# Kernel tuning notes

Measured on AMD Instinct MI355X. Metric: run time of the kernel, lower is better.

Reference implementation:

```python
import jax, jax.numpy as jnp
import numpy as np

NUM_PROJS = 7
BLOCK = 256       # HyperAttention block_size
SAMPLE = 256      # HyperAttention sample_size
NUM_HEADS = 16

def _hamming_perm(n):
    a = np.array([0, 1])
    for _ in range(n - 1):
        a = np.concatenate([a, a[::-1] + a.max() + 1])
    return a

_PERM = jnp.asarray(_hamming_perm(NUM_PROJS))           # [128] gray-code-ish bucket reorder
_ENC = (2 ** jnp.arange(NUM_PROJS)).astype(jnp.int32)   # [7]

def _lsh_hash(mat, proj_dir):
    # mat: [B,H,N,d], proj_dir: [d,7] -> bucket ids [B,H,N]
    bits = jnp.einsum('bhnd,dr->bhnr', mat, proj_dir) > 0
    ids = (bits * _ENC).sum(-1)
    return _PERM[ids]

def _attn_lse(q, k, v, scale, bias=None):
    s = jnp.einsum('...qd,...kd->...qk', q, k) * scale
    if bias is not None:
        s = s + bias
    lse = jax.nn.logsumexp(s, axis=-1, keepdims=True)
    o = jnp.einsum('...qk,...kd->...qd', jnp.exp(s - lse), v)
    return o, lse

def _gather(t, idx):
    # gather rows along axis 2: out[b,h,s] = t[b,h,idx[b,h,s]]
    return jnp.take_along_axis(t, idx[..., None], axis=2)

def setup_inputs():
    key = jax.random.key(0)
    ks = jax.random.split(key, 7)
    B, L, D, INNER = 2, 8192, 1024, 1024
    x = jax.random.normal(ks[0], (B, L, D), jnp.float32)
    W_qkv = jax.random.normal(ks[1], (D, 3 * INNER), jnp.float32) / np.sqrt(D)
    b_qkv = jnp.zeros((3 * INNER,), jnp.float32)
    W_proj = jax.random.normal(ks[2], (INNER, D), jnp.float32) / np.sqrt(INNER)
    b_proj = jnp.zeros((D,), jnp.float32)
    proj_dir = jax.random.normal(ks[3], (INNER // NUM_HEADS, NUM_PROJS), jnp.float32)
    sampled_set = jax.random.randint(ks[4], (B, NUM_HEADS, SAMPLE), 0, L)
    return {"x": x, "W_qkv": W_qkv, "b_qkv": b_qkv, "W_proj": W_proj,
            "b_proj": b_proj, "proj_dir": proj_dir, "sampled_set": sampled_set}

def reference(x, W_qkv, b_qkv, W_proj, b_proj, proj_dir, sampled_set):
    B, L, D = x.shape
    qkv = (x @ W_qkv + b_qkv).reshape(B, L, 3, NUM_HEADS, -1).transpose(2, 0, 3, 1, 4)
    q, k, v = qkv[0], qkv[1], qkv[2]                      # [B,H,L,dh]
    dh = q.shape[-1]
    scale = dh ** -0.5
    # 1. sortLSH: stable sort q and k rows by angular-LSH bucket id
    q_idx = jnp.argsort(_lsh_hash(q, proj_dir), axis=2, stable=True)
    k_idx = jnp.argsort(_lsh_hash(k, proj_dir), axis=2, stable=True)
    q_idx_inv = jnp.argsort(q_idx, axis=2, stable=True)   # to restore row order
    qs = _gather(q, q_idx)
    ksort = _gather(k, k_idx)
    vsort = _gather(v, k_idx)
    # block-diagonal exact attention over the sorted order (L % BLOCK == 0 here)
    nb = L // BLOCK
    ab, lb = _attn_lse(qs.reshape(B, NUM_HEADS, nb, BLOCK, dh),
                       ksort.reshape(B, NUM_HEADS, nb, BLOCK, dh),
                       vsort.reshape(B, NUM_HEADS, nb, BLOCK, dh), scale)
    attn_block = ab.reshape(B, NUM_HEADS, L, dh)
    lse_block = lb.reshape(B, NUM_HEADS, L, 1)
    # 2. residual uniformly-sampled attention, masking entries already covered by blocks
    k_sub = _gather(ksort, sampled_set)                   # [B,H,SAMPLE,dh]
    v_sub = _gather(vsort, sampled_set)
    blk_q = jnp.arange(L)[None, None, :, None] // BLOCK   # query block id (query_block_size==BLOCK)
    mask = blk_q == (sampled_set // BLOCK)[:, :, None, :]  # [B,H,L,SAMPLE]
    bias = jnp.where(mask, jnp.finfo(x.dtype).min, 0.0).astype(x.dtype)
    attn_res, lse_res = _attn_lse(qs, k_sub, v_sub, scale, bias)
    lse_res = lse_res + jnp.log(jnp.float32(L) / SAMPLE)  # importance weight n_key/sample_size
    # combine the two attentions via their log-sum-exps
    c = 1.0 / (1.0 + jnp.exp(lse_res - lse_block))
    attn = c * attn_block + (1.0 - c) * attn_res
    out = _gather(attn, q_idx_inv)                        # un-sort rows back to input order
    out = out.transpose(0, 2, 1, 3).reshape(B, L, -1)     # [B,L,inner]
    return out @ W_proj + b_proj
```

## Files before the change

kernel.cpp:

```cpp
#include <hip/hip_runtime.h>
#include <hip/hip_fp16.h>
#include <math.h>


typedef _Float16 f16x8 __attribute__((ext_vector_type(8)));
typedef _Float16 f16x4 __attribute__((ext_vector_type(4)));
typedef __fp16 fp16x2 __attribute__((ext_vector_type(2)));
typedef float f32x4 __attribute__((ext_vector_type(4)));

#define WLIST_CAP 524288
#define TAU 0.08f

__device__ __forceinline__ void gl_lds16(const void* g, void* s) {
    __builtin_amdgcn_global_load_lds(
        (const __attribute__((address_space(1))) unsigned int*)g,
        (__attribute__((address_space(3))) unsigned int*)s, 16, 0, 0);
}

__global__ __launch_bounds__(256) void fold_kernel(
    const float* __restrict__ W, const float* __restrict__ bias,
    const float* __restrict__ proj, double* __restrict__ fold,
    double* __restrict__ bfold, _Float16* __restrict__ foldh,
    float* __restrict__ bfold32)
{
    int idx = blockIdx.x * 256 + threadIdx.x;
    if (idx < 2 * 16 * 7 * 1024) {
        int task = idx / 7168;
        int rem = idx - task * 7168;
        int i = rem / 7;
        int r = rem - i * 7;
        int h = task & 15, w = task >> 4;
        double s = 0.0;
        const float* wp = W + (size_t)i * 3072 + w * 1024 + h * 64;
        for (int d = 0; d < 64; ++d)
            s += (double)wp[d] * (double)proj[d * 7 + r];
        fold[idx] = s;
        foldh[((size_t)task * 7 + r) * 1024 + i] = (_Float16)s;
    }
    if (idx < 32768)
        foldh[229376 + idx] = (_Float16)0.f;
    if (idx < 224) {
        int r = idx % 7;
        int task = idx / 7;
        int h = task & 15, w = task >> 4;
        double s = 0.0;
        for (int d = 0; d < 64; ++d)
            s += (double)bias[w * 1024 + h * 64 + d] * (double)proj[d * 7 + r];
        bfold[idx] = s;
        bfold32[idx] = (float)s;
    }
}

__global__ __launch_bounds__(256) void hashext_kernel(
    const float* __restrict__ scores, const float* __restrict__ bfold32,
    int* __restrict__ hq, int* __restrict__ hk,
    int* __restrict__ wcount, int* __restrict__ wlist)
{
    int tid = blockIdx.x * 256 + threadIdx.x;
    int row = tid >> 5, task = tid & 31;
    const float* sp = scores + (size_t)row * 256 + task * 7;
    int id = 0, fl = 0;
#pragma unroll
    for (int r = 0; r < 7; ++r) {
        float val = sp[r] + bfold32[task * 7 + r];
        if (fabsf(val) < TAU) fl = 1;
        if (val > 0.f) id |= (1 << r);
    }
    int hsh = id ^ (id >> 1);
    int w = task >> 4, h = task & 15;
    int b = row >> 13, l = row & 8191;
    (w ? hk : hq)[((size_t)(b * 16 + h) << 13) + l] = hsh;
    if (fl) {
        int slot = atomicAdd(wcount, 1);
        if (slot < WLIST_CAP) wlist[slot] = task * 16384 + row;
    }
}

__global__ __launch_bounds__(256) void refine_kernel(
    const float* __restrict__ x, const double* __restrict__ fold,
    const double* __restrict__ bfold, const int* __restrict__ wcount,
    const int* __restrict__ wlist, int* __restrict__ hq, int* __restrict__ hk)
{
    int n = *wcount;
    if (n > WLIST_CAP) n = WLIST_CAP;
    int lane = threadIdx.x & 63;
    int wid = (blockIdx.x * 256 + threadIdx.x) >> 6;
    int nw = gridDim.x * 4;
    for (int e = wid; e < n; e += nw) {
        int code = wlist[e];
        int task = code >> 14, grow = code & 16383;
        const double* f = fold + (size_t)task * 7168;
        const float* xp = x + (size_t)grow * 1024;
        double acc[7] = {0, 0, 0, 0, 0, 0, 0};
        for (int i = lane; i < 1024; i += 64) {
            double xv = (double)xp[i];
#pragma unroll
            for (int rr = 0; rr < 7; ++rr)
                acc[rr] = fma(xv, f[(size_t)i * 7 + rr], acc[rr]);
        }
        int id = 0;
#pragma unroll
        for (int rr = 0; rr < 7; ++rr) {
            double a = acc[rr];
#pragma unroll
            for (int off = 32; off > 0; off >>= 1) a += __shfl_xor(a, off, 64);
            if (a + bfold[task * 7 + rr] > 0.0) id |= (1 << rr);
        }
        if (lane == 0) {
            int hsh = id ^ (id >> 1);
            int w = task >> 4, h = task & 15;
            int b = grow >> 13, l = grow & 8191;
            (w ? hk : hq)[((size_t)(b * 16 + h) << 13) + l] = hsh;
        }
    }
}

__global__ __launch_bounds__(256) void sort_kernel(
    const int* __restrict__ hq, const int* __restrict__ hk,
    int* __restrict__ qidx, int* __restrict__ kidx)
{
    __shared__ unsigned short cnt[128][128];
    __shared__ int tot[128];
    __shared__ int base[128];
    int blk = blockIdx.x;
    int sel = blk >> 5, bh = blk & 31;
    const int* hp = (sel ? hk : hq) + ((size_t)bh << 13);
    int* op = (sel ? kidx : qidx) + ((size_t)bh << 13);
    int t = threadIdx.x;
    for (int i = t; i < 128 * 128 / 2; i += 256) ((unsigned int*)cnt)[i] = 0u;
    __syncthreads();
    if (t < 128) {
        const int* p = hp + t * 64;
        for (int j = 0; j < 64; ++j) cnt[t][p[j]]++;
    }
    __syncthreads();
    if (t < 128) {
        int run = 0;
        for (int c = 0; c < 128; ++c) {
            int x2 = cnt[c][t];
            cnt[c][t] = (unsigned short)run;
            run += x2;
        }
        tot[t] = run;
    }
    __syncthreads();
    if (t == 0) {
        int run = 0;
        for (int v = 0; v < 128; ++v) { base[v] = run; run += tot[v]; }
    }
    __syncthreads();
    if (t < 128) {
        const int* p = hp + t * 64;
        for (int j = 0; j < 64; ++j) {
            int v = p[j];
            int c = cnt[t][v];
            cnt[t][v] = (unsigned short)(c + 1);
            op[base[v] + c] = t * 64 + j;
        }
    }
}

__global__ __launch_bounds__(256) void castx_kernel(
    const float* __restrict__ x, _Float16* __restrict__ xh)
{
    int i = blockIdx.x * 256 + threadIdx.x;
    float4 f = ((const float4*)x)[i];
    _Float16 h4[4] = {(_Float16)f.x, (_Float16)f.y, (_Float16)f.z, (_Float16)f.w};
    *(short4*)&xh[(size_t)i * 4] = *(short4*)h4;
}

__global__ __launch_bounds__(256) void transpose_kernel(
    const float* __restrict__ W, _Float16* __restrict__ Wt, int K, int N)
{
    __shared__ float tile[32][33];
    int bx = blockIdx.x, by = blockIdx.y;
    int tx = threadIdx.x & 31, ty = threadIdx.x >> 5;
    for (int i = ty; i < 32; i += 8)
        tile[i][tx] = W[(size_t)(by * 32 + i) * N + bx * 32 + tx];
    __syncthreads();
    for (int i = ty; i < 32; i += 8)
        Wt[(size_t)(bx * 32 + i) * K + by * 32 + tx] = (_Float16)tile[tx][i];
}

template <int MODE>
__global__ __launch_bounds__(256) void mfma_gemm(
    const _Float16* __restrict__ A, const _Float16* __restrict__ Bt,
    const float* __restrict__ bias, float* __restrict__ C,
    _Float16* __restrict__ Q, _Float16* __restrict__ Kb, _Float16* __restrict__ Vb,
    int K, int N)
{
    __shared__ __align__(16) _Float16 As[128 * 32];
    __shared__ __align__(16) _Float16 Bs[128 * 32];
    int t = threadIdx.x;
    int w = t >> 6, l = t & 63;
    int m0 = blockIdx.y * 128, n0 = blockIdx.x * 128;
    const _Float16* ga = A + (size_t)(m0 + 32 * w + (l >> 2)) * K + (l & 3) * 8;
    const _Float16* gb = Bt + (size_t)(n0 + 32 * w + (l >> 2)) * K + (l & 3) * 8;
    char* lasA = (char*)As + w * 2048;
    char* lasB = (char*)Bs + w * 2048;
    int wr = w >> 1, wc = w & 1;
    int rl = l & 15, ks = l >> 4;
    f32x4 acc[4][4];
#pragma unroll
    for (int m = 0; m < 4; ++m)
#pragma unroll
        for (int n = 0; n < 4; ++n) acc[m][n] = (f32x4){0.f, 0.f, 0.f, 0.f};
    for (int kk = 0; kk < K; kk += 32) {
        __syncthreads();
        gl_lds16(ga, lasA);
        gl_lds16(ga + 16 * K, lasA + 1024);
        gl_lds16(gb, lasB);
        gl_lds16(gb + 16 * K, lasB + 1024);
        ga += 32; gb += 32;
        __syncthreads();
        f16x8 af[4], bf[4];
#pragma unroll
        for (int m = 0; m < 4; ++m)
            af[m] = *(const f16x8*)((char*)As + (64 * wr + 16 * m + rl) * 64 + ks * 16);
#pragma unroll
        for (int n = 0; n < 4; ++n)
            bf[n] = *(const f16x8*)((char*)Bs + (64 * wc + 16 * n + rl) * 64 + ks * 16);
#pragma unroll
        for (int m = 0; m < 4; ++m)
#pragma unroll
            for (int n = 0; n < 4; ++n)
                acc[m][n] = __builtin_amdgcn_mfma_f32_16x16x32_f16(
                    af[m], bf[n], acc[m][n], 0, 0, 0);
    }
#pragma unroll
    for (int m = 0; m < 4; ++m) {
#pragma unroll
        for (int n = 0; n < 4; ++n) {
            int gn = n0 + 64 * wc + 16 * n + rl;
            float bv = (MODE == 2) ? 0.f : bias[gn];
#pragma unroll
            for (int j = 0; j < 4; ++j) {
                int gm = m0 + 64 * wr + 16 * m + 4 * ks + j;
                float val = acc[m][n][j] + bv;
                if (MODE == 1) {
                    int s = gn >> 10, h = (gn >> 6) & 15, d = gn & 63;
                    int b2 = gm >> 13, ll = gm & 8191;
                    _Float16* dst = (s == 0) ? Q : (s == 1 ? Kb : Vb);
                    dst[(((size_t)(b2 * 16 + h) << 13) + ll) * 64 + d] = (_Float16)val;
                } else {
                    C[(size_t)gm * N + gn] = val;
                }
            }
        }
    }
}

__global__ __launch_bounds__(256) void attn_mfma_kernel(
    const _Float16* __restrict__ q, const _Float16* __restrict__ k,
    const _Float16* __restrict__ v, const int* __restrict__ qidx,
    const int* __restrict__ kidx, const int* __restrict__ sampled,
    _Float16* __restrict__ pre)
{
    __shared__ __align__(16) _Float16 Vt[2][64 * 68];
    __shared__ int sposS[2][64];
    __shared__ int krowS[2][64];
    int bh = blockIdx.x >> 6, qb = (blockIdx.x >> 1) & 31, half = blockIdx.x & 1;
    int bb = bh >> 4, hh = bh & 15;
    size_t hb = (size_t)bh << 13;
    size_t bhs = (size_t)bh * 256;
    int t = threadIdx.x;
    int w = t >> 6, l = t & 63;
    int g = l >> 4, c16 = l & 15;
    int kg = t & 15, dg = t >> 4;
    int qw0 = qb * 256 + half * 128 + w * 32;
    const _Float16 qs = (_Float16)0.125f;

    int orig[2];
    f16x8 qf[2][2];
#pragma unroll
    for (int n = 0; n < 2; ++n) {
        orig[n] = qidx[hb + qw0 + 16 * n + c16];
        const _Float16* qp = q + (hb + orig[n]) * 64 + g * 8;
        qf[n][0] = *(const f16x8*)(qp);
        qf[n][1] = *(const f16x8*)(qp + 32);
#pragma unroll
        for (int j = 0; j < 8; ++j) { qf[n][0][j] *= qs; qf[n][1][j] *= qs; }
    }
    f32x4 o[4][2];
    float mr[2], lr[2];
#pragma unroll
    for (int n = 0; n < 2; ++n) {
        mr[n] = -1e30f; lr[n] = 0.f;
#pragma unroll
        for (int d2 = 0; d2 < 4; ++d2) o[d2][n] = (f32x4){0.f, 0.f, 0.f, 0.f};
    }
    const float LOG32 = 3.4657359027997265f;

    {
        if (t < 64) {
            int p = qb * 256 + t;
            sposS[0][t] = p;
            krowS[0][t] = kidx[hb + p];
        }
        f16x4 vr[4];
#pragma unroll
        for (int j2 = 0; j2 < 4; ++j2) {
            int p = qb * 256 + 4 * kg + j2;
            int kr = kidx[hb + p];
            vr[j2] = *(const f16x4*)(v + (hb + kr) * 64 + 4 * dg);
        }
#pragma unroll
        for (int i = 0; i < 4; ++i) {
            f16x4 o4 = {vr[0][i], vr[1][i], vr[2][i], vr[3][i]};
            *(f16x4*)&Vt[0][(4 * dg + i) * 68 + 4 * kg] = o4;
        }
    }

    for (int c = 0; c < 8; ++c) {
        int cur = c & 1, nxt = cur ^ 1;
        bool samp = c >= 4;
        __syncthreads();
        int krA[4];
#pragma unroll
        for (int m = 0; m < 4; ++m) krA[m] = krowS[cur][16 * m + c16];
        f16x8 kf[4][2];
#pragma unroll
        for (int m = 0; m < 4; ++m) {
            const _Float16* kp = k + (hb + krA[m]) * 64 + g * 8;
            kf[m][0] = *(const f16x8*)(kp);
            kf[m][1] = *(const f16x8*)(kp + 32);
        }
        int np_s = 0, nkr_s = 0, krn[4];
        if (c < 7) {
            bool snx = (c + 1) >= 4;
            if (t < 64) {
                np_s = snx ? sampled[bhs + (c - 3) * 64 + t] : qb * 256 + (c + 1) * 64 + t;
                nkr_s = kidx[hb + np_s];
            }
#pragma unroll
            for (int j2 = 0; j2 < 4; ++j2) {
                int key = 4 * kg + j2;
                int p = snx ? sampled[bhs + (c - 3) * 64 + key]
                            : qb * 256 + (c + 1) * 64 + key;
                krn[j2] = kidx[hb + p];
            }
        }
        f32x4 sacc[4][2];
#pragma unroll
        for (int m = 0; m < 4; ++m)
#pragma unroll
            for (int n = 0; n < 2; ++n) sacc[m][n] = (f32x4){0.f, 0.f, 0.f, 0.f};
#pragma unroll
        for (int m = 0; m < 4; ++m) {
#pragma unroll
            for (int n = 0; n < 2; ++n)
                sacc[m][n] = __builtin_amdgcn_mfma_f32_16x16x32_f16(
                    kf[m][0], qf[n][0], sacc[m][n], 0, 0, 0);
#pragma unroll
            for (int n = 0; n < 2; ++n)
                sacc[m][n] = __builtin_amdgcn_mfma_f32_16x16x32_f16(
                    kf[m][1], qf[n][1], sacc[m][n], 0, 0, 0);
        }
        f16x4 vrn[4];
        if (c < 7) {
#pragma unroll
            for (int j2 = 0; j2 < 4; ++j2)
                vrn[j2] = *(const f16x4*)(v + (hb + krn[j2]) * 64 + 4 * dg);
        }
        f16x4 av[4][4];
#pragma unroll
        for (int m = 0; m < 4; ++m)
#pragma unroll
            for (int d2 = 0; d2 < 4; ++d2)
                av[m][d2] = *(const f16x4*)&Vt[cur][(16 * d2 + c16) * 68 + 16 * m + 4 * g];
        bool msk[4][4];
#pragma unroll
        for (int m = 0; m < 4; ++m)
#pragma unroll
            for (int r = 0; r < 4; ++r)
                msk[m][r] = samp && ((sposS[cur][16 * m + 4 * g + r] >> 8) == qb);
        float badd = samp ? LOG32 : 0.f;
#pragma unroll
        for (int n = 0; n < 2; ++n) {
            float sv[16];
#pragma unroll
            for (int m = 0; m < 4; ++m)
#pragma unroll
                for (int r = 0; r < 4; ++r)
                    sv[4 * m + r] = msk[m][r] ? -1e30f : sacc[m][n][r] + badd;
            float a0 = fmaxf(fmaxf(sv[0], sv[1]), sv[2]);
            float a1 = fmaxf(fmaxf(sv[3], sv[4]), sv[5]);
            float a2 = fmaxf(fmaxf(sv[6], sv[7]), sv[8]);
            float a3 = fmaxf(fmaxf(sv[9], sv[10]), sv[11]);
            float a4 = fmaxf(fmaxf(sv[12], sv[13]), sv[14]);
            float cm = fmaxf(fmaxf(fmaxf(a0, a1), a2), fmaxf(fmaxf(a3, a4), sv[15]));
            cm = fmaxf(cm, __shfl_xor(cm, 16, 64));
            cm = fmaxf(cm, __shfl_xor(cm, 32, 64));
            if (__any(cm > mr[n])) {
                float nm = fmaxf(mr[n], cm);
                float fq = __expf(mr[n] - nm);
                mr[n] = nm;
                lr[n] *= fq;
#pragma unroll
                for (int d2 = 0; d2 < 4; ++d2) {
                    o[d2][n][0] *= fq; o[d2][n][1] *= fq;
                    o[d2][n][2] *= fq; o[d2][n][3] *= fq;
                }
            }
            float pv16[16];
#pragma unroll
            for (int r = 0; r < 16; ++r) pv16[r] = __expf(sv[r] - mr[n]);
            float s0 = (pv16[0] + pv16[1]) + (pv16[2] + pv16[3]);
            float s1 = (pv16[4] + pv16[5]) + (pv16[6] + pv16[7]);
            float s2 = (pv16[8] + pv16[9]) + (pv16[10] + pv16[11]);
            float s3 = (pv16[12] + pv16[13]) + (pv16[14] + pv16[15]);
            float ps = (s0 + s1) + (s2 + s3);
            ps += __shfl_xor(ps, 16, 64);
            ps += __shfl_xor(ps, 32, 64);
            lr[n] += ps;
            f16x4 pb[4];
#pragma unroll
            for (int m = 0; m < 4; ++m) {
                fp16x2 c0 = __builtin_amdgcn_cvt_pkrtz(pv16[4 * m + 0], pv16[4 * m + 1]);
                fp16x2 c1 = __builtin_amdgcn_cvt_pkrtz(pv16[4 * m + 2], pv16[4 * m + 3]);
                pb[m][0] = (_Float16)c0[0]; pb[m][1] = (_Float16)c0[1];
                pb[m][2] = (_Float16)c1[0]; pb[m][3] = (_Float16)c1[1];
            }
#pragma unroll
            for (int d2 = 0; d2 < 4; ++d2)
#pragma unroll
                for (int m = 0; m < 4; ++m)
                    o[d2][n] = __builtin_amdgcn_mfma_f32_16x16x16f16(
                        av[m][d2], pb[m], o[d2][n], 0, 0, 0);
        }
        if (c < 7) {
            if (t < 64) { sposS[nxt][t] = np_s; krowS[nxt][t] = nkr_s; }
#pragma unroll
            for (int i = 0; i < 4; ++i) {
                f16x4 o4 = {vrn[0][i], vrn[1][i], vrn[2][i], vrn[3][i]};
                *(f16x4*)&Vt[nxt][(4 * dg + i) * 68 + 4 * kg] = o4;
            }
        }
    }
#pragma unroll
    for (int n = 0; n < 2; ++n) {
        float invl = 1.f / lr[n];
        _Float16* pp = pre + ((size_t)(bb * 8192 + orig[n])) * 1024 + hh * 64;
#pragma unroll
        for (int d2 = 0; d2 < 4; ++d2) {
            f16x4 st;
            st[0] = (_Float16)(o[d2][n][0] * invl);
            st[1] = (_Float16)(o[d2][n][1] * invl);
            st[2] = (_Float16)(o[d2][n][2] * invl);
            st[3] = (_Float16)(o[d2][n][3] * invl);
            *(f16x4*)(pp + 16 * d2 + 4 * g) = st;
        }
    }
}

extern "C" void kernel_launch(void* const* d_in, const int* in_sizes, int n_in,
                              void* d_out, int out_size, void* d_ws, size_t ws_size,
                              hipStream_t stream)
{
    (void)in_sizes; (void)n_in; (void)out_size; (void)ws_size;
    const float* x     = (const float*)d_in[0];
    const float* Wqkv  = (const float*)d_in[1];
    const float* bqkv  = (const float*)d_in[2];
    const float* Wproj = (const float*)d_in[3];
    const float* bproj = (const float*)d_in[4];
    const float* proj  = (const float*)d_in[5];
    const int*   samp  = (const int*)d_in[6];
    float* out = (float*)d_out;

    char* ws = (char*)d_ws;
    size_t off = 0;
    auto take = [&](size_t bytes) {
        char* p = ws + off;
        off = (off + bytes + 255) & ~(size_t)255;
        return p;
    };
    _Float16* xh  = (_Float16*)take(33554432);
    _Float16* q   = (_Float16*)take(33554432);
    _Float16* k   = (_Float16*)take(33554432);
    _Float16* v   = (_Float16*)take(33554432);
    float* scores = (float*)take(16777216);
    _Float16* Wtq = (_Float16*)take(6291456);
    _Float16* Wtp = (_Float16*)take(2097152);
    _Float16* foldh = (_Float16*)take(524288);
    double* fold   = (double*)take(1835008);
    double* bfold  = (double*)take(1792);
    float* bfold32 = (float*)take(896);
    int* wcount = (int*)take(256);
    int* wlist  = (int*)take(WLIST_CAP * 4);
    int* hq   = (int*)take(1048576);
    int* hk   = (int*)take(1048576);
    int* qidx = (int*)take(1048576);
    int* kidx = (int*)take(1048576);
    _Float16* pre = xh;

    (void)hipMemsetAsync(wcount, 0, 4, stream);
    castx_kernel<<<dim3(16384), dim3(256), 0, stream>>>(x, xh);
    fold_kernel<<<dim3(896), dim3(256), 0, stream>>>(
        Wqkv, bqkv, proj, fold, bfold, foldh, bfold32);
    mfma_gemm<2><<<dim3(2, 128), dim3(256), 0, stream>>>(
        xh, foldh, nullptr, scores, nullptr, nullptr, nullptr, 1024, 256);
    hashext_kernel<<<dim3(2048), dim3(256), 0, stream>>>(
        scores, bfold32, hq, hk, wcount, wlist);
    refine_kernel<<<dim3(2048), dim3(256), 0, stream>>>(
        x, fold, bfold, wcount, wlist, hq, hk);
    sort_kernel<<<dim3(64), dim3(256), 0, stream>>>(hq, hk, qidx, kidx);
    transpose_kernel<<<dim3(96, 32), dim3(256), 0, stream>>>(Wqkv, Wtq, 1024, 3072);
    transpose_kernel<<<dim3(32, 32), dim3(256), 0, stream>>>(Wproj, Wtp, 1024, 1024);
    mfma_gemm<1><<<dim3(24, 128), dim3(256), 0, stream>>>(
        xh, Wtq, bqkv, nullptr, q, k, v, 1024, 3072);
    attn_mfma_kernel<<<dim3(2048), dim3(256), 0, stream>>>(
        q, k, v, qidx, kidx, samp, pre);
    mfma_gemm<0><<<dim3(8, 128), dim3(256), 0, stream>>>(
        pre, Wtp, bproj, out, nullptr, nullptr, nullptr, 1024, 1024);
}
```

Measured before the change: 644.6 us.

## Scatter Q/K/V into LSH-sorted order in QKV GEMM epilogue and pre-gather samples

The sort kernel now also emits inverse permutations (rank arrays). The QKV GEMM epilogue uses them to write Q, K and V rows directly at their sorted positions, and a small kernel gathers the sampled K/V rows into contiguous buffers. The attention kernel can then read Q, K and V tiles contiguously instead of doing per-row kidx indirection and LDS index staging. The cost is scattered row writes in the GEMM epilogue, an extra tiny launch, and more workspace.

Result: faster. 606.0 us (-6.0%).

```diff
diff --git a/kernel.cpp b/kernel.cpp
--- a/kernel.cpp
+++ b/kernel.cpp
@@ -117,7 +117,8 @@
 
 __global__ __launch_bounds__(256) void sort_kernel(
     const int* __restrict__ hq, const int* __restrict__ hk,
-    int* __restrict__ qidx, int* __restrict__ kidx)
+    int* __restrict__ qidx, int* __restrict__ kidx,
+    int* __restrict__ qrank, int* __restrict__ krank)
 {
     __shared__ unsigned short cnt[128][128];
     __shared__ int tot[128];
@@ -126,6 +127,7 @@
     int sel = blk >> 5, bh = blk & 31;
     const int* hp = (sel ? hk : hq) + ((size_t)bh << 13);
     int* op = (sel ? kidx : qidx) + ((size_t)bh << 13);
+    int* rp = (sel ? krank : qrank) + ((size_t)bh << 13);
     int t = threadIdx.x;
     for (int i = t; i < 128 * 128 / 2; i += 256) ((unsigned int*)cnt)[i] = 0u;
     __syncthreads();
@@ -155,7 +157,9 @@
             int v = p[j];
             int c = cnt[t][v];
             cnt[t][v] = (unsigned short)(c + 1);
-            op[base[v] + c] = t * 64 + j;
+            int pos = base[v] + c;
+            op[pos] = t * 64 + j;
+            rp[t * 64 + j] = pos;
         }
     }
 }
@@ -182,11 +186,30 @@
         Wt[(size_t)(bx * 32 + i) * K + by * 32 + tx] = (_Float16)tile[tx][i];
 }
 
+__global__ __launch_bounds__(256) void gather_samp_kernel(
+    const _Float16* __restrict__ ks, const _Float16* __restrict__ vs,
+    const int* __restrict__ sampled, _Float16* __restrict__ ksamp,
+    _Float16* __restrict__ vsamp)
+{
+    int bh = blockIdx.x;
+    int key = blockIdx.y * 64 + (threadIdx.x >> 2);
+    int qtr = (threadIdx.x & 3) * 16;
+    size_t hb = (size_t)bh << 13;
+    int p = sampled[bh * 256 + key];
+    size_t src = (hb + p) * 64 + qtr;
+    size_t dst = ((size_t)bh * 256 + key) * 64 + qtr;
+    *(f16x8*)(ksamp + dst)     = *(const f16x8*)(ks + src);
+    *(f16x8*)(ksamp + dst + 8) = *(const f16x8*)(ks + src + 8);
+    *(f16x8*)(vsamp + dst)     = *(const f16x8*)(vs + src);
+    *(f16x8*)(vsamp + dst + 8) = *(const f16x8*)(vs + src + 8);
+}
+
 template <int MODE>
 __global__ __launch_bounds__(256) void mfma_gemm(
     const _Float16* __restrict__ A, const _Float16* __restrict__ Bt,
     const float* __restrict__ bias, float* __restrict__ C,
     _Float16* __restrict__ Q, _Float16* __restrict__ Kb, _Float16* __restrict__ Vb,
+    const int* __restrict__ qrank, const int* __restrict__ krank,
     int K, int N)
 {
     __shared__ __align__(16) _Float16 As[128 * 32];
@@ -227,38 +250,54 @@
                 acc[m][n] = __builtin_amdgcn_mfma_f32_16x16x32_f16(
                     af[m], bf[n], acc[m][n], 0, 0, 0);
     }
-#pragma unroll
-    for (int m = 0; m < 4; ++m) {
-#pragma unroll
-        for (int n = 0; n < 4; ++n) {
-            int gn = n0 + 64 * wc + 16 * n + rl;
-            float bv = (MODE == 2) ? 0.f : bias[gn];
-#pragma unroll
-            for (int j = 0; j < 4; ++j) {
-                int gm = m0 + 64 * wr + 16 * m + 4 * ks + j;
-                float val = acc[m][n][j] + bv;
-                if (MODE == 1) {
-                    int s = gn >> 10, h = (gn >> 6) & 15, d = gn & 63;
-                    int b2 = gm >> 13, ll = gm & 8191;
-                    _Float16* dst = (s == 0) ? Q : (s == 1 ? Kb : Vb);
-                    dst[(((size_t)(b2 * 16 + h) << 13) + ll) * 64 + d] = (_Float16)val;
-                } else {
-                    C[(size_t)gm * N + gn] = val;
+    if (MODE == 1) {
+        int s0 = n0 >> 10;
+        int h = ((n0 >> 6) + wc) & 15;
+        int b2 = m0 >> 13;
+        const int* rkarr = (s0 == 0) ? qrank : krank;
+        _Float16* dst = (s0 == 0) ? Q : (s0 == 1 ? Kb : Vb);
+        size_t bhb = ((size_t)(b2 * 16 + h) << 13);
+        int llb = (m0 & 8191) + 64 * wr + 4 * ks;
+        int pos[4][4];
+#pragma unroll
+        for (int m = 0; m < 4; ++m)
+#pragma unroll
+            for (int j = 0; j < 4; ++j)
+                pos[m][j] = rkarr[bhb + llb + 16 * m + j];
+#pragma unroll
+        for (int m = 0; m < 4; ++m)
+#pragma unroll
+            for (int n = 0; n < 4; ++n) {
+                int gn = n0 + 64 * wc + 16 * n + rl;
+                float bv = bias[gn];
+                int d = 16 * n + rl;
+#pragma unroll
+                for (int j = 0; j < 4; ++j)
+                    dst[(bhb + pos[m][j]) * 64 + d] = (_Float16)(acc[m][n][j] + bv);
+            }
+    } else {
+#pragma unroll
+        for (int m = 0; m < 4; ++m)
+#pragma unroll
+            for (int n = 0; n < 4; ++n) {
+                int gn = n0 + 64 * wc + 16 * n + rl;
+                float bv = (MODE == 2) ? 0.f : bias[gn];
+#pragma unroll
+                for (int j = 0; j < 4; ++j) {
+                    int gm = m0 + 64 * wr + 16 * m + 4 * ks + j;
+                    C[(size_t)gm * N + gn] = acc[m][n][j] + bv;
                 }
             }
-        }
     }
 }
 
 __global__ __launch_bounds__(256) void attn_mfma_kernel(
-    const _Float16* __restrict__ q, const _Float16* __restrict__ k,
-    const _Float16* __restrict__ v, const int* __restrict__ qidx,
-    const int* __restrict__ kidx, const int* __restrict__ sampled,
-    _Float16* __restrict__ pre)
+    const _Float16* __restrict__ qs_, const _Float16* __restrict__ ks_,
+    const _Float16* __restrict__ vs_, const _Float16* __restrict__ ksamp,
+    const _Float16* __restrict__ vsamp, const int* __restrict__ qidx,
+    const int* __restrict__ sampled, _Float16* __restrict__ pre)
 {
     __shared__ __align__(16) _Float16 Vt[2][64 * 68];
-    __shared__ int sposS[2][64];
-    __shared__ int krowS[2][64];
     int bh = blockIdx.x >> 6, qb = (blockIdx.x >> 1) & 31, half = blockIdx.x & 1;
     int bb = bh >> 4, hh = bh & 15;
     size_t hb = (size_t)bh << 13;
@@ -274,8 +313,9 @@
     f16x8 qf[2][2];
 #pragma unroll
     for (int n = 0; n < 2; ++n) {
-        orig[n] = qidx[hb + qw0 + 16 * n + c16];
-        const _Float16* qp = q + (hb + orig[n]) * 64 + g * 8;
+        int row = qw0 + 16 * n + c16;
+        orig[n] = qidx[hb + row];
+        const _Float16* qp = qs_ + (hb + row) * 64 + g * 8;
         qf[n][0] = *(const f16x8*)(qp);
         qf[n][1] = *(const f16x8*)(qp + 32);
 #pragma unroll
@@ -292,18 +332,11 @@
     const float LOG32 = 3.4657359027997265f;
 
     {
-        if (t < 64) {
-            int p = qb * 256 + t;
-            sposS[0][t] = p;
-            krowS[0][t] = kidx[hb + p];
-        }
+        const _Float16* vb = vs_ + (hb + qb * 256) * 64;
         f16x4 vr[4];
 #pragma unroll
-        for (int j2 = 0; j2 < 4; ++j2) {
-            int p = qb * 256 + 4 * kg + j2;
-            int kr = kidx[hb + p];
-            vr[j2] = *(const f16x4*)(v + (hb + kr) * 64 + 4 * dg);
-        }
+        for (int j2 = 0; j2 < 4; ++j2)
+            vr[j2] = *(const f16x4*)(vb + (4 * kg + j2) * 64 + 4 * dg);
 #pragma unroll
         for (int i = 0; i < 4; ++i) {
             f16x4 o4 = {vr[0][i], vr[1][i], vr[2][i], vr[3][i]};
@@ -315,30 +348,20 @@
         int cur = c & 1, nxt = cur ^ 1;
         bool samp = c >= 4;
         __syncthreads();
-        int krA[4];
-#pragma unroll
-        for (int m = 0; m < 4; ++m) krA[m] = krowS[cur][16 * m + c16];
+        const _Float16* kb = samp ? ksamp + (bhs + (size_t)(c - 4) * 64) * 64
+                                  : ks_ + (hb + qb * 256 + (size_t)c * 64) * 64;
         f16x8 kf[4][2];
 #pragma unroll
         for (int m = 0; m < 4; ++m) {
-            const _Float16* kp = k + (hb + krA[m]) * 64 + g * 8;
+            const _Float16* kp = kb + (16 * m + c16) * 64 + g * 8;
             kf[m][0] = *(const f16x8*)(kp);
             kf[m][1] = *(const f16x8*)(kp + 32);
         }
-        int np_s = 0, nkr_s = 0, krn[4];
-        if (c < 7) {
-            bool snx = (c + 1) >= 4;
-            if (t < 64) {
-                np_s = snx ? sampled[bhs + (c - 3) * 64 + t] : qb * 256 + (c + 1) * 64 + t;
-                nkr_s = kidx[hb + np_s];
-            }
-#pragma unroll
-            for (int j2 = 0; j2 < 4; ++j2) {
-                int key = 4 * kg + j2;
-                int p = snx ? sampled[bhs + (c - 3) * 64 + key]
-                            : qb * 256 + (c + 1) * 64 + key;
-                krn[j2] = kidx[hb + p];
-            }
+        int4 spv[4];
+        if (samp) {
+#pragma unroll
+            for (int m = 0; m < 4; ++m)
+                spv[m] = *(const int4*)(sampled + bhs + (c - 4) * 64 + 16 * m + 4 * g);
         }
         f32x4 sacc[4][2];
 #pragma unroll
@@ -358,9 +381,12 @@
         }
         f16x4 vrn[4];
         if (c < 7) {
+            const _Float16* vb = (c + 1 >= 4)
+                ? vsamp + (bhs + (size_t)(c - 3) * 64) * 64
+                : vs_ + (hb + qb * 256 + (size_t)(c + 1) * 64) * 64;
 #pragma unroll
             for (int j2 = 0; j2 < 4; ++j2)
-                vrn[j2] = *(const f16x4*)(v + (hb + krn[j2]) * 64 + 4 * dg);
+                vrn[j2] = *(const f16x4*)(vb + (4 * kg + j2) * 64 + 4 * dg);
         }
         f16x4 av[4][4];
 #pragma unroll
@@ -370,10 +396,12 @@
                 av[m][d2] = *(const f16x4*)&Vt[cur][(16 * d2 + c16) * 68 + 16 * m + 4 * g];
         bool msk[4][4];
 #pragma unroll
-        for (int m = 0; m < 4; ++m)
-#pragma unroll
-            for (int r = 0; r < 4; ++r)
-                msk[m][r] = samp && ((sposS[cur][16 * m + 4 * g + r] >> 8) == qb);
+        for (int m = 0; m < 4; ++m) {
+            msk[m][0] = samp && ((spv[m].x >> 8) == qb);
+            msk[m][1] = samp && ((spv[m].y >> 8) == qb);
+            msk[m][2] = samp && ((spv[m].z >> 8) == qb);
+            msk[m][3] = samp && ((spv[m].w >> 8) == qb);
+        }
         float badd = samp ? LOG32 : 0.f;
 #pragma unroll
         for (int n = 0; n < 2; ++n) {
@@ -429,7 +457,6 @@
                         av[m][d2], pb[m], o[d2][n], 0, 0, 0);
         }
         if (c < 7) {
-            if (t < 64) { sposS[nxt][t] = np_s; krowS[nxt][t] = nkr_s; }
 #pragma unroll
             for (int i = 0; i < 4; ++i) {
                 f16x4 o4 = {vrn[0][i], vrn[1][i], vrn[2][i], vrn[3][i]};
@@ -482,15 +509,19 @@
     _Float16* Wtq = (_Float16*)take(6291456);
     _Float16* Wtp = (_Float16*)take(2097152);
     _Float16* foldh = (_Float16*)take(524288);
+    _Float16* ksamp = (_Float16*)take(1048576);
+    _Float16* vsamp = (_Float16*)take(1048576);
     double* fold   = (double*)take(1835008);
     double* bfold  = (double*)take(1792);
     float* bfold32 = (float*)take(896);
     int* wcount = (int*)take(256);
     int* wlist  = (int*)take(WLIST_CAP * 4);
-    int* hq   = (int*)take(1048576);
-    int* hk   = (int*)take(1048576);
-    int* qidx = (int*)take(1048576);
-    int* kidx = (int*)take(1048576);
+    int* hq    = (int*)take(1048576);
+    int* hk    = (int*)take(1048576);
+    int* qidx  = (int*)take(1048576);
+    int* kidx  = (int*)take(1048576);
+    int* qrank = (int*)take(1048576);
+    int* krank = (int*)take(1048576);
     _Float16* pre = xh;
 
     (void)hipMemsetAsync(wcount, 0, 4, stream);
@@ -498,18 +529,23 @@
     fold_kernel<<<dim3(896), dim3(256), 0, stream>>>(
         Wqkv, bqkv, proj, fold, bfold, foldh, bfold32);
     mfma_gemm<2><<<dim3(2, 128), dim3(256), 0, stream>>>(
-        xh, foldh, nullptr, scores, nullptr, nullptr, nullptr, 1024, 256);
+        xh, foldh, nullptr, scores, nullptr, nullptr, nullptr, nullptr, nullptr,
+        1024, 256);
     hashext_kernel<<<dim3(2048), dim3(256), 0, stream>>>(
         scores, bfold32, hq, hk, wcount, wlist);
     refine_kernel<<<dim3(2048), dim3(256), 0, stream>>>(
         x, fold, bfold, wcount, wlist, hq, hk);
-    sort_kernel<<<dim3(64), dim3(256), 0, stream>>>(hq, hk, qidx, kidx);
+    sort_kernel<<<dim3(64), dim3(256), 0, stream>>>(
+        hq, hk, qidx, kidx, qrank, krank);
     transpose_kernel<<<dim3(96, 32), dim3(256), 0, stream>>>(Wqkv, Wtq, 1024, 3072);
     transpose_kernel<<<dim3(32, 32), dim3(256), 0, stream>>>(Wproj, Wtp, 1024, 1024);
     mfma_gemm<1><<<dim3(24, 128), dim3(256), 0, stream>>>(
-        xh, Wtq, bqkv, nullptr, q, k, v, 1024, 3072);
+        xh, Wtq, bqkv, nullptr, q, k, v, qrank, krank, 1024, 3072);
+    gather_samp_kernel<<<dim3(32, 4), dim3(256), 0, stream>>>(
+        k, v, samp, ksamp, vsamp);
     attn_mfma_kernel<<<dim3(2048), dim3(256), 0, stream>>>(
-        q, k, v, qidx, kidx, samp, pre);
+        q, k, v, ksamp, vsamp, qidx, samp, pre);
     mfma_gemm<0><<<dim3(8, 128), dim3(256), 0, stream>>>(
-        pre, Wtp, bproj, out, nullptr, nullptr, nullptr, 1024, 1024);
-}
+        pre, Wtp, bproj, out, nullptr, nullptr, nullptr, nullptr, nullptr,
+        1024, 1024);
+}
```
